# Kernel optimization log

Measured on AMD Instinct MI355X. Metric: run time of the kernel, lower is better.

The kernel has to match this reference:

```python
import jax, jax.numpy as jnp
import numpy as np

VAR_CXCY = 0.1   # variances[0]
VAR_WH = 0.2     # variances[1]
MIN_OVERLAP = 0.5
NEG_POS_RATIO = 3


def cxcy_to_xyxy(b):
    return jnp.concatenate([b[:, :2] - b[:, 2:] / 2, b[:, :2] + b[:, 2:] / 2], axis=-1)


def jaccard(a, b):
    # a: [O,4] xyxy, b: [P,4] xyxy -> [O,P]
    lt = jnp.maximum(a[:, None, :2], b[None, :, :2])
    rb = jnp.minimum(a[:, None, 2:], b[None, :, 2:])
    wh = jnp.clip(rb - lt, 0.0)
    inter = wh[..., 0] * wh[..., 1]
    area_a = (a[:, 2] - a[:, 0]) * (a[:, 3] - a[:, 1])
    area_b = (b[:, 2] - b[:, 0]) * (b[:, 3] - b[:, 1])
    return inter / (area_a[:, None] + area_b[None, :] - inter)


def xyxy_to_gcxgcy(boxes, priors):
    # boxes: [P,4] xyxy matched per-prior; priors: [P,4] cxcywh
    cxcy = (boxes[:, :2] + boxes[:, 2:]) / 2
    wh = boxes[:, 2:] - boxes[:, :2]
    g_cxcy = (cxcy - priors[:, :2]) / (priors[:, 2:] * VAR_CXCY)
    g_wh = jnp.log(wh / priors[:, 2:]) / VAR_WH
    return jnp.concatenate([g_cxcy, g_wh], axis=-1)


def _match_one(boxes, labels, priors, priors_xyxy):
    # boxes: [O,4] xyxy, labels: [O] int
    overlaps = jaccard(boxes, priors_xyxy)          # [O,P]
    prior_overlaps = overlaps.max(axis=0)            # [P]
    prior_objects = overlaps.argmax(axis=0)          # [P]
    object_priors = overlaps.argmax(axis=1)          # [O] best prior per object
    n_obj = boxes.shape[0]
    prior_objects = prior_objects.at[object_priors].set(jnp.arange(n_obj))
    prior_overlaps = prior_overlaps.at[object_priors].set(1.0)
    lab = labels[prior_objects]
    lab = jnp.where(prior_overlaps < MIN_OVERLAP, 0, lab)
    locs = xyxy_to_gcxgcy(boxes[prior_objects], priors)
    return locs, lab


def setup_inputs() -> dict:
    key = jax.random.key(0)
    B, P, C, O = 64, 8732, 81, 16
    ks = jax.random.split(key, 6)
    predict_locs = jax.random.normal(ks[0], (B, P, 4), dtype=jnp.float32)
    predict_confs = jax.random.normal(ks[1], (B, P, C), dtype=jnp.float32)
    # priors in cxcywh, valid sizes
    p_cxcy = jax.random.uniform(ks[2], (P, 2), minval=0.0, maxval=1.0)
    p_wh = jax.random.uniform(ks[2], (P, 2), minval=0.05, maxval=0.3)
    priors = jnp.concatenate([p_cxcy, p_wh], axis=-1).astype(jnp.float32)
    # targets: valid xyxy boxes in [0,1]
    t_cxcy = jax.random.uniform(ks[3], (B, O, 2), minval=0.2, maxval=0.8)
    t_wh = jax.random.uniform(ks[4], (B, O, 2), minval=0.05, maxval=0.4)
    target_boxes = jnp.concatenate([t_cxcy - t_wh / 2, t_cxcy + t_wh / 2], axis=-1).astype(jnp.float32)
    target_labels = jax.random.randint(ks[5], (B, O), 1, C)
    return {
        'predict_locs': predict_locs,
        'predict_confs': predict_confs,
        'target_boxes': target_boxes,
        'target_labels': target_labels,
        'priors': priors,
    }


def reference(predict_locs, predict_confs, target_boxes, target_labels, priors):
    priors_xyxy = cxcy_to_xyxy(priors)
    true_locs, true_confs = jax.vmap(
        lambda b, l: _match_one(b, l, priors, priors_xyxy)
    )(target_boxes, target_labels)              # [B,P,4], [B,P]

    pos = true_confs != 0                        # [B,P]
    n_pos = pos.sum(axis=1)                      # [B]
    n_pos_total = n_pos.sum().astype(predict_locs.dtype)

    # nn.L1Loss(reduction='mean') over the [n_pos_total, 4] gathered entries
    loc_loss = jnp.sum(jnp.abs(predict_locs - true_locs) * pos[..., None]) / (n_pos_total * 4)

    logp = jax.nn.log_softmax(predict_confs, axis=-1)
    ce = -jnp.take_along_axis(logp, true_confs[..., None], axis=-1)[..., 0]  # [B,P]

    ce_pos_sum = jnp.sum(jnp.where(pos, ce, 0.0))
    ce_neg = jnp.where(pos, 0.0, ce)
    # double-sort rank: rank of each prior when sorted by descending neg loss
    rank = jnp.argsort(jnp.argsort(-ce_neg, axis=1), axis=1)
    hard = rank < (NEG_POS_RATIO * n_pos)[:, None]
    ce_hard_sum = jnp.sum(jnp.where(hard, ce_neg, 0.0))

    conf_loss = (ce_hard_sum + ce_pos_sum) / n_pos_total
    return conf_loss + loc_loss
```

## Files before the change

kernel.cpp:

```cpp
#include <hip/hip_runtime.h>
#include <cstdint>
#include <cstddef>

constexpr int O_C   = 16;
constexpr int P_MAX = 8732;
constexpr int CH    = 4;
constexpr int CHP   = 2183;

struct f4u { float x, y, z, w; };

__device__ __forceinline__ float waveSumF(float v) {
    #pragma unroll
    for (int off = 32; off; off >>= 1) v += __shfl_xor(v, off);
    return v;
}
__device__ __forceinline__ int waveSumI(int v) {
    #pragma unroll
    for (int off = 32; off; off >>= 1) v += __shfl_xor(v, off);
    return v;
}

__global__ __launch_bounds__(256) void matchA1(
    const float* __restrict__ target_boxes,
    const float* __restrict__ priors,
    float* __restrict__ ov_out,
    unsigned char* __restrict__ obj_out,
    unsigned long long* __restrict__ okey_part,
    int P)
{
    const int b    = blockIdx.x / CH;
    const int c    = blockIdx.x % CH;
    const int tid  = threadIdx.x;
    const int lane = tid & 63;
    const int wid  = tid >> 6;

    __shared__ float bx0[O_C], by0[O_C], bx1[O_C], by1[O_C], barea[O_C];
    __shared__ unsigned long long s_wb[O_C * 4];

    if (tid < O_C) {
        const float* tb = target_boxes + ((size_t)b * O_C + tid) * 4;
        float x0 = tb[0], y0 = tb[1], x1 = tb[2], y1 = tb[3];
        bx0[tid] = x0; by0[tid] = y0; bx1[tid] = x1; by1[tid] = y1;
        barea[tid] = (x1 - x0) * (y1 - y0);
    }
    __syncthreads();

    float bi[O_C]; int bp[O_C];
    #pragma unroll
    for (int o = 0; o < O_C; ++o) { bi[o] = -1.0f; bp[o] = 0; }

    const int p0 = c * CHP, p1 = min(p0 + CHP, P);
    for (int p = p0 + tid; p < p1; p += 256) {
        float4 pr = reinterpret_cast<const float4*>(priors)[p];
        float px0 = pr.x - pr.z * 0.5f, py0 = pr.y - pr.w * 0.5f;
        float px1 = pr.x + pr.z * 0.5f, py1 = pr.y + pr.w * 0.5f;
        float parea = (px1 - px0) * (py1 - py0);
        float bv = -1.0f; int bo = 0;
        #pragma unroll
        for (int o = 0; o < O_C; ++o) {
            float ix0 = fmaxf(px0, bx0[o]), iy0 = fmaxf(py0, by0[o]);
            float ix1 = fminf(px1, bx1[o]), iy1 = fminf(py1, by1[o]);
            float iw = fmaxf(ix1 - ix0, 0.0f), ih = fmaxf(iy1 - iy0, 0.0f);
            float inter = iw * ih;
            float iou = inter / (barea[o] + parea - inter);
            if (iou > bv) { bv = iou; bo = o; }
            if (iou > bi[o]) { bi[o] = iou; bp[o] = p; }
        }
        ov_out[(size_t)b * P + p]  = bv;
        obj_out[(size_t)b * P + p] = (unsigned char)bo;
    }

    #pragma unroll
    for (int o = 0; o < O_C; ++o) {
        unsigned long long k = (bi[o] >= 0.0f)
            ? (((unsigned long long)__float_as_uint(bi[o]) << 32) |
               (unsigned long long)(0xFFFFFFFFu - (unsigned)bp[o]))
            : 0ull;
        #pragma unroll
        for (int off = 32; off; off >>= 1) {
            unsigned long long k2 = __shfl_xor(k, off);
            if (k2 > k) k = k2;
        }
        if (lane == 0) s_wb[o * 4 + wid] = k;
    }
    __syncthreads();
    if (tid < O_C) {
        unsigned long long k = s_wb[tid * 4];
        #pragma unroll
        for (int w = 1; w < 4; ++w) if (s_wb[tid * 4 + w] > k) k = s_wb[tid * 4 + w];
        okey_part[(size_t)blockIdx.x * O_C + tid] = k;
    }
}

__global__ __launch_bounds__(256) void ce_stream(
    const float* __restrict__ confs,
    const float* __restrict__ ov_in,
    const unsigned char* __restrict__ obj_in,
    const unsigned long long* __restrict__ okey_part,
    const float* __restrict__ target_boxes,
    const int*   __restrict__ target_labels,
    const float* __restrict__ priors,
    const float* __restrict__ predict_locs,
    float* __restrict__ ce_out,
    float* __restrict__ loc_part,
    int P, int rows)
{
    const int tid  = threadIdx.x;
    const int lane = tid & 63;
    const int wid  = tid >> 6;
    const int row0 = blockIdx.x * 256;
    const int row  = row0 + tid;

    __shared__ float4 tbox[2][O_C];
    __shared__ int    tlab[2][O_C], topr[2][O_C];
    __shared__ float  s_facc[4];

    const int b0     = row0 / P;
    const int rsplit = min(row0 + 256, (b0 + 1) * P);
    const int b1     = (rsplit < row0 + 256) ? b0 + 1 : b0;

    if (tid < 2 * O_C) {
        const int seg = tid >> 4, o = tid & 15;
        const int bb  = seg ? b1 : b0;
        const float* tb = target_boxes + ((size_t)bb * O_C + o) * 4;
        tbox[seg][o] = make_float4(tb[0], tb[1], tb[2], tb[3]);
        tlab[seg][o] = target_labels[(size_t)bb * O_C + o];
        unsigned long long kk = 0ull;
        #pragma unroll
        for (int cc = 0; cc < CH; ++cc) {
            unsigned long long k2 = okey_part[((size_t)bb * CH + cc) * O_C + o];
            if (k2 > kk) kk = k2;
        }
        topr[seg][o] = (int)(0xFFFFFFFFu - (unsigned)(kk & 0xFFFFFFFFull));
    }
    __syncthreads();

    const float* rbase = confs + (size_t)row * 81;
    const f4u* rp = reinterpret_cast<const f4u*>(rbase);
    float m = -3.0e38f, s = 0.0f;
    #pragma unroll
    for (int j = 0; j < 20; ++j) {
        f4u a = rp[j];
        float m4 = fmaxf(fmaxf(a.x, a.y), fmaxf(a.z, a.w));
        float mn = fmaxf(m, m4);
        s = s * __expf(m - mn)
          + __expf(a.x - mn) + __expf(a.y - mn)
          + __expf(a.z - mn) + __expf(a.w - mn);
        m = mn;
    }
    {
        float last = rbase[80];
        float mn = fmaxf(m, last);
        s = s * __expf(m - mn) + __expf(last - mn);
        m = mn;
    }

    const int seg = (row >= rsplit) ? 1 : 0;
    const int bb  = seg ? b1 : b0;
    const int p   = row - bb * P;
    float ovv = ov_in[row];
    int   obj = obj_in[row];
    #pragma unroll
    for (int o = 0; o < O_C; ++o)
        if (topr[seg][o] == p) { obj = o; ovv = 1.0f; }
    const int l = (ovv < 0.5f) ? 0 : tlab[seg][obj];

    float xl  = rbase[l];
    float cev = m + __logf(s) - xl;
    ce_out[row] = l ? -cev : cev;

    float locacc = 0.0f;
    if (l) {
        float4 pr = reinterpret_cast<const float4*>(priors)[p];
        float4 tb = tbox[seg][obj];
        float cx = (tb.x + tb.z) * 0.5f, cy = (tb.y + tb.w) * 0.5f;
        float w  = tb.z - tb.x,          h  = tb.w - tb.y;
        float g0 = (cx - pr.x) / (pr.z * 0.1f);
        float g1 = (cy - pr.y) / (pr.w * 0.1f);
        float g2 = logf(w / pr.z) / 0.2f;
        float g3 = logf(h / pr.w) / 0.2f;
        float4 pl = reinterpret_cast<const float4*>(predict_locs)[row];
        locacc = fabsf(pl.x - g0) + fabsf(pl.y - g1) +
                 fabsf(pl.z - g2) + fabsf(pl.w - g3);
    }
    float a = waveSumF(locacc);
    if (lane == 0) s_facc[wid] = a;
    __syncthreads();
    if (tid == 0)
        loc_part[blockIdx.x] = s_facc[0] + s_facc[1] + s_facc[2] + s_facc[3];
}

__global__ __launch_bounds__(1024) void hard_kernel(
    const float* __restrict__ ce,
    int*   __restrict__ n_pos,
    float* __restrict__ ce_pos,
    float* __restrict__ ce_hard,
    int P)
{
    const int b    = blockIdx.x;
    const int tid  = threadIdx.x;
    const int lane = tid & 63;
    const int wid  = tid >> 6;

    __shared__ float s_v[P_MAX];
    __shared__ unsigned int hist[16][256];
    __shared__ unsigned int s_sel;
    __shared__ int s_kr;
    __shared__ float s_f[16], s_f2[16];
    __shared__ int s_i[16];

    const size_t base = (size_t)b * P;
    float possum = 0.0f, negsum = 0.0f;
    int cnt = 0;
    for (int p = tid; p < P; p += 1024) {
        float c = ce[base + p];
        unsigned u = __float_as_uint(c);
        float sv;
        if (u >> 31) { possum += -c; ++cnt; sv = 0.0f; }
        else         { negsum += c;         sv = c;    }
        s_v[p] = sv;
    }
    possum = waveSumF(possum);
    negsum = waveSumF(negsum);
    cnt    = waveSumI(cnt);
    if (lane == 0) { s_f[wid] = possum; s_f2[wid] = negsum; s_i[wid] = cnt; }
    __syncthreads();
    float negsum_t = 0.0f, possum_t = 0.0f; int np = 0;
    #pragma unroll
    for (int w = 0; w < 16; ++w) { negsum_t += s_f2[w]; possum_t += s_f[w]; np += s_i[w]; }
    if (tid == 0) { ce_pos[b] = possum_t; n_pos[b] = np; }

    const int K = 3 * np;
    if (K <= 0) { if (tid == 0) ce_hard[b] = 0.0f; return; }
    if (K >= P) { if (tid == 0) ce_hard[b] = negsum_t; return; }

    unsigned int prefix = 0; int kr = K;
    for (int shift = 24; shift >= 0; shift -= 8) {
        for (int i = tid; i < 16 * 256; i += 1024) (&hist[0][0])[i] = 0;
        __syncthreads();
        unsigned int maskHi = (shift == 24) ? 0u : (0xFFFFFFFFu << (shift + 8));
        for (int p = tid; p < P; p += 1024) {
            unsigned int u = __float_as_uint(s_v[p]);
            if ((u & maskHi) == prefix) atomicAdd(&hist[wid][(u >> shift) & 255], 1u);
        }
        __syncthreads();
        if (wid == 0) {
            unsigned h0 = 0, h1 = 0, h2 = 0, h3 = 0;
            #pragma unroll 4
            for (int w = 0; w < 16; ++w) {
                h0 += hist[w][lane * 4 + 0];
                h1 += hist[w][lane * 4 + 1];
                h2 += hist[w][lane * 4 + 2];
                h3 += hist[w][lane * 4 + 3];
            }
            unsigned own = h0 + h1 + h2 + h3;
            unsigned t = own;
            #pragma unroll
            for (int off = 1; off < 64; off <<= 1) {
                unsigned u = __shfl_down(t, off);
                if (lane + off >= 64) u = 0;
                t += u;
            }
            unsigned Tnext = t - own;
            unsigned cum3 = Tnext;
            unsigned cum2 = cum3 + h3;
            unsigned cum1 = cum2 + h2;
            unsigned cum0 = cum1 + h1;
            unsigned kru = (unsigned)kr;
            int selj = -1; unsigned cg = 0;
            if      (cum3 < kru && kru <= cum3 + h3) { selj = 3; cg = cum3; }
            else if (cum2 < kru && kru <= cum2 + h2) { selj = 2; cg = cum2; }
            else if (cum1 < kru && kru <= cum1 + h1) { selj = 1; cg = cum1; }
            else if (cum0 < kru && kru <= cum0 + h0) { selj = 0; cg = cum0; }
            if (selj >= 0) {
                s_sel = prefix | ((unsigned)(lane * 4 + selj) << shift);
                s_kr  = kr - (int)cg;
            }
        }
        __syncthreads();
        prefix = s_sel; kr = s_kr;
        __syncthreads();
    }

    float sumgt = 0.0f;
    for (int p = tid; p < P; p += 1024) {
        unsigned int u = __float_as_uint(s_v[p]);
        if (u > prefix) sumgt += s_v[p];
    }
    sumgt = waveSumF(sumgt);
    if (lane == 0) s_f[wid] = sumgt;
    __syncthreads();
    if (tid == 0) {
        float sg = 0.0f;
        #pragma unroll
        for (int w = 0; w < 16; ++w) sg += s_f[w];
        ce_hard[b] = sg + (float)kr * __uint_as_float(prefix);
    }
}

__global__ __launch_bounds__(256) void finalize_kernel(
    const int*   __restrict__ n_pos,
    const float* __restrict__ ce_pos,
    const float* __restrict__ ce_hard,
    const float* __restrict__ loc_part,
    float* __restrict__ out, int B, int nblk)
{
    __shared__ float s_f[4];
    __shared__ float s_res[3];
    const int tid  = threadIdx.x;
    const int lane = tid & 63;
    const int wid  = tid >> 6;

    float la = 0.0f;
    for (int i = tid; i < nblk; i += 256) la += loc_part[i];
    la = waveSumF(la);
    if (lane == 0) s_f[wid] = la;

    if (tid < 64) {
        int np = 0; float cp = 0.0f, ch = 0.0f;
        for (int b = lane; b < B; b += 64) {
            np += n_pos[b]; cp += ce_pos[b]; ch += ce_hard[b];
        }
        #pragma unroll
        for (int off = 32; off; off >>= 1) {
            np += __shfl_xor(np, off);
            cp += __shfl_xor(cp, off);
            ch += __shfl_xor(ch, off);
        }
        if (lane == 0) {
            s_res[0] = (float)np; s_res[1] = cp; s_res[2] = ch;
        }
    }
    __syncthreads();
    if (tid == 0) {
        float latot = s_f[0] + s_f[1] + s_f[2] + s_f[3];
        float npt = s_res[0];
        out[0] = (s_res[2] + s_res[1]) / npt + latot / (npt * 4.0f);
    }
}

extern "C" void kernel_launch(void* const* d_in, const int* in_sizes, int n_in,
                              void* d_out, int out_size, void* d_ws, size_t ws_size,
                              hipStream_t stream) {
    const float* predict_locs  = (const float*)d_in[0];
    const float* predict_confs = (const float*)d_in[1];
    const float* target_boxes  = (const float*)d_in[2];
    const int*   target_labels = (const int*)d_in[3];
    const float* priors        = (const float*)d_in[4];

    const int P = in_sizes[4] / 4;
    const int B = in_sizes[0] / (P * 4);
    const int rows = B * P;
    const int nblk = rows / 256;

    char* ws = (char*)d_ws;
    unsigned long long* okey_part = (unsigned long long*)ws;
    ws += (size_t)B * CH * O_C * sizeof(unsigned long long);
    float* ce      = (float*)ws; ws += (size_t)rows * sizeof(float);
    float* ov      = (float*)ws; ws += (size_t)rows * sizeof(float);
    float* loc_p   = (float*)ws; ws += (size_t)nblk * sizeof(float);
    int*   n_pos   = (int*)ws;   ws += (size_t)B * sizeof(int);
    float* ce_pos  = (float*)ws; ws += (size_t)B * sizeof(float);
    float* ce_hard = (float*)ws; ws += (size_t)B * sizeof(float);
    unsigned char* obj = (unsigned char*)ws; ws += (size_t)rows;

    matchA1<<<B * CH, 256, 0, stream>>>(target_boxes, priors, ov, obj, okey_part, P);
    ce_stream<<<nblk, 256, 0, stream>>>(predict_confs, ov, obj, okey_part,
                                        target_boxes, target_labels, priors,
                                        predict_locs, ce, loc_p, P, rows);
    hard_kernel<<<B, 1024, 0, stream>>>(ce, n_pos, ce_pos, ce_hard, P);
    finalize_kernel<<<1, 256, 0, stream>>>(n_pos, ce_pos, ce_hard, loc_p,
                                           (float*)d_out, B, rows / 256);
}
```

Measured before the change: 78.32 us.

## Fuse matching with logsumexp stream and move label/loc work into hard kernel

The prior-matching blocks and the per-row logsumexp blocks now run in one launch, since the logsumexp no longer depends on the match results. Label resolution, the target-logit gather, positive CE and the L1 loc loss move into the per-batch hard-mining kernel, which removes one launch and the serial dependency between matching and the heavy confidence stream. The cost is that the 64-block hard kernel now does scattered gathers from confs and predict_locs, so its low parallelism may lengthen that kernel.

```diff
diff --git a/kernel.cpp b/kernel.cpp
--- a/kernel.cpp
+++ b/kernel.cpp
@@ -20,17 +20,47 @@
     return v;
 }
 
-__global__ __launch_bounds__(256) void matchA1(
+__global__ __launch_bounds__(256, 4) void fused_stream(
+    const float* __restrict__ confs,
     const float* __restrict__ target_boxes,
     const float* __restrict__ priors,
     float* __restrict__ ov_out,
     unsigned char* __restrict__ obj_out,
     unsigned long long* __restrict__ okey_part,
-    int P)
+    float* __restrict__ lse_out,
+    int P, int rows, int nmatch)
 {
-    const int b    = blockIdx.x / CH;
-    const int c    = blockIdx.x % CH;
     const int tid  = threadIdx.x;
+
+    if (blockIdx.x >= nmatch) {
+        const int row = (blockIdx.x - nmatch) * 256 + tid;
+        if (row >= rows) return;
+        const float* rbase = confs + (size_t)row * 81;
+        const f4u* rp = reinterpret_cast<const f4u*>(rbase);
+        float m = -3.0e38f, s = 0.0f;
+        #pragma unroll
+        for (int j = 0; j < 20; ++j) {
+            f4u a = rp[j];
+            float m4 = fmaxf(fmaxf(a.x, a.y), fmaxf(a.z, a.w));
+            float mn = fmaxf(m, m4);
+            s = s * __expf(m - mn)
+              + __expf(a.x - mn) + __expf(a.y - mn)
+              + __expf(a.z - mn) + __expf(a.w - mn);
+            m = mn;
+        }
+        {
+            float last = rbase[80];
+            float mn = fmaxf(m, last);
+            s = s * __expf(m - mn) + __expf(last - mn);
+            m = mn;
+        }
+        lse_out[row] = m + __logf(s);
+        return;
+    }
+
+    const int chunk = blockIdx.x;
+    const int b    = chunk / CH;
+    const int c    = chunk % CH;
     const int lane = tid & 63;
     const int wid  = tid >> 6;
 
@@ -88,12 +118,13 @@
         unsigned long long k = s_wb[tid * 4];
         #pragma unroll
         for (int w = 1; w < 4; ++w) if (s_wb[tid * 4 + w] > k) k = s_wb[tid * 4 + w];
-        okey_part[(size_t)blockIdx.x * O_C + tid] = k;
-    }
-}
-
-__global__ __launch_bounds__(256) void ce_stream(
+        okey_part[(size_t)chunk * O_C + tid] = k;
+    }
+}
+
+__global__ __launch_bounds__(1024) void hard_kernel(
     const float* __restrict__ confs,
+    const float* __restrict__ lse,
     const float* __restrict__ ov_in,
     const unsigned char* __restrict__ obj_in,
     const unsigned long long* __restrict__ okey_part,
@@ -101,100 +132,10 @@
     const int*   __restrict__ target_labels,
     const float* __restrict__ priors,
     const float* __restrict__ predict_locs,
-    float* __restrict__ ce_out,
-    float* __restrict__ loc_part,
-    int P, int rows)
-{
-    const int tid  = threadIdx.x;
-    const int lane = tid & 63;
-    const int wid  = tid >> 6;
-    const int row0 = blockIdx.x * 256;
-    const int row  = row0 + tid;
-
-    __shared__ float4 tbox[2][O_C];
-    __shared__ int    tlab[2][O_C], topr[2][O_C];
-    __shared__ float  s_facc[4];
-
-    const int b0     = row0 / P;
-    const int rsplit = min(row0 + 256, (b0 + 1) * P);
-    const int b1     = (rsplit < row0 + 256) ? b0 + 1 : b0;
-
-    if (tid < 2 * O_C) {
-        const int seg = tid >> 4, o = tid & 15;
-        const int bb  = seg ? b1 : b0;
-        const float* tb = target_boxes + ((size_t)bb * O_C + o) * 4;
-        tbox[seg][o] = make_float4(tb[0], tb[1], tb[2], tb[3]);
-        tlab[seg][o] = target_labels[(size_t)bb * O_C + o];
-        unsigned long long kk = 0ull;
-        #pragma unroll
-        for (int cc = 0; cc < CH; ++cc) {
-            unsigned long long k2 = okey_part[((size_t)bb * CH + cc) * O_C + o];
-            if (k2 > kk) kk = k2;
-        }
-        topr[seg][o] = (int)(0xFFFFFFFFu - (unsigned)(kk & 0xFFFFFFFFull));
-    }
-    __syncthreads();
-
-    const float* rbase = confs + (size_t)row * 81;
-    const f4u* rp = reinterpret_cast<const f4u*>(rbase);
-    float m = -3.0e38f, s = 0.0f;
-    #pragma unroll
-    for (int j = 0; j < 20; ++j) {
-        f4u a = rp[j];
-        float m4 = fmaxf(fmaxf(a.x, a.y), fmaxf(a.z, a.w));
-        float mn = fmaxf(m, m4);
-        s = s * __expf(m - mn)
-          + __expf(a.x - mn) + __expf(a.y - mn)
-          + __expf(a.z - mn) + __expf(a.w - mn);
-        m = mn;
-    }
-    {
-        float last = rbase[80];
-        float mn = fmaxf(m, last);
-        s = s * __expf(m - mn) + __expf(last - mn);
-        m = mn;
-    }
-
-    const int seg = (row >= rsplit) ? 1 : 0;
-    const int bb  = seg ? b1 : b0;
-    const int p   = row - bb * P;
-    float ovv = ov_in[row];
-    int   obj = obj_in[row];
-    #pragma unroll
-    for (int o = 0; o < O_C; ++o)
-        if (topr[seg][o] == p) { obj = o; ovv = 1.0f; }
-    const int l = (ovv < 0.5f) ? 0 : tlab[seg][obj];
-
-    float xl  = rbase[l];
-    float cev = m + __logf(s) - xl;
-    ce_out[row] = l ? -cev : cev;
-
-    float locacc = 0.0f;
-    if (l) {
-        float4 pr = reinterpret_cast<const float4*>(priors)[p];
-        float4 tb = tbox[seg][obj];
-        float cx = (tb.x + tb.z) * 0.5f, cy = (tb.y + tb.w) * 0.5f;
-        float w  = tb.z - tb.x,          h  = tb.w - tb.y;
-        float g0 = (cx - pr.x) / (pr.z * 0.1f);
-        float g1 = (cy - pr.y) / (pr.w * 0.1f);
-        float g2 = logf(w / pr.z) / 0.2f;
-        float g3 = logf(h / pr.w) / 0.2f;
-        float4 pl = reinterpret_cast<const float4*>(predict_locs)[row];
-        locacc = fabsf(pl.x - g0) + fabsf(pl.y - g1) +
-                 fabsf(pl.z - g2) + fabsf(pl.w - g3);
-    }
-    float a = waveSumF(locacc);
-    if (lane == 0) s_facc[wid] = a;
-    __syncthreads();
-    if (tid == 0)
-        loc_part[blockIdx.x] = s_facc[0] + s_facc[1] + s_facc[2] + s_facc[3];
-}
-
-__global__ __launch_bounds__(1024) void hard_kernel(
-    const float* __restrict__ ce,
     int*   __restrict__ n_pos,
     float* __restrict__ ce_pos,
     float* __restrict__ ce_hard,
+    float* __restrict__ loc_b,
     int P)
 {
     const int b    = blockIdx.x;
@@ -204,31 +145,70 @@
 
     __shared__ float s_v[P_MAX];
     __shared__ unsigned int hist[16][256];
+    __shared__ float4 tbox[O_C];
+    __shared__ int    tlab[O_C], topr[O_C];
     __shared__ unsigned int s_sel;
     __shared__ int s_kr;
-    __shared__ float s_f[16], s_f2[16];
+    __shared__ float s_f[16], s_f2[16], s_f3[16];
     __shared__ int s_i[16];
 
+    if (tid < O_C) {
+        const float* tb = target_boxes + ((size_t)b * O_C + tid) * 4;
+        tbox[tid] = make_float4(tb[0], tb[1], tb[2], tb[3]);
+        tlab[tid] = target_labels[(size_t)b * O_C + tid];
+        unsigned long long kk = 0ull;
+        #pragma unroll
+        for (int cc = 0; cc < CH; ++cc) {
+            unsigned long long k2 = okey_part[((size_t)b * CH + cc) * O_C + tid];
+            if (k2 > kk) kk = k2;
+        }
+        topr[tid] = (int)(0xFFFFFFFFu - (unsigned)(kk & 0xFFFFFFFFull));
+    }
+    __syncthreads();
+
     const size_t base = (size_t)b * P;
-    float possum = 0.0f, negsum = 0.0f;
+    float possum = 0.0f, negsum = 0.0f, locsum = 0.0f;
     int cnt = 0;
     for (int p = tid; p < P; p += 1024) {
-        float c = ce[base + p];
-        unsigned u = __float_as_uint(c);
-        float sv;
-        if (u >> 31) { possum += -c; ++cnt; sv = 0.0f; }
-        else         { negsum += c;         sv = c;    }
-        s_v[p] = sv;
+        float ovv = ov_in[base + p];
+        int   obj = obj_in[base + p];
+        #pragma unroll
+        for (int o = 0; o < O_C; ++o)
+            if (topr[o] == p) { obj = o; ovv = 1.0f; }
+        const int l = (ovv < 0.5f) ? 0 : tlab[obj];
+        float xl  = confs[(base + p) * 81 + l];
+        float cev = lse[base + p] - xl;
+        if (l != 0) {
+            possum += cev; ++cnt;
+            s_v[p] = 0.0f;
+            float4 pr = reinterpret_cast<const float4*>(priors)[p];
+            float4 tb = tbox[obj];
+            float cx = (tb.x + tb.z) * 0.5f, cy = (tb.y + tb.w) * 0.5f;
+            float w  = tb.z - tb.x,          h  = tb.w - tb.y;
+            float g0 = (cx - pr.x) / (pr.z * 0.1f);
+            float g1 = (cy - pr.y) / (pr.w * 0.1f);
+            float g2 = logf(w / pr.z) / 0.2f;
+            float g3 = logf(h / pr.w) / 0.2f;
+            float4 pl = reinterpret_cast<const float4*>(predict_locs)[base + p];
+            locsum += fabsf(pl.x - g0) + fabsf(pl.y - g1) +
+                      fabsf(pl.z - g2) + fabsf(pl.w - g3);
+        } else {
+            negsum += cev;
+            s_v[p] = cev;
+        }
     }
     possum = waveSumF(possum);
     negsum = waveSumF(negsum);
+    locsum = waveSumF(locsum);
     cnt    = waveSumI(cnt);
-    if (lane == 0) { s_f[wid] = possum; s_f2[wid] = negsum; s_i[wid] = cnt; }
-    __syncthreads();
-    float negsum_t = 0.0f, possum_t = 0.0f; int np = 0;
-    #pragma unroll
-    for (int w = 0; w < 16; ++w) { negsum_t += s_f2[w]; possum_t += s_f[w]; np += s_i[w]; }
-    if (tid == 0) { ce_pos[b] = possum_t; n_pos[b] = np; }
+    if (lane == 0) { s_f[wid] = possum; s_f2[wid] = negsum; s_f3[wid] = locsum; s_i[wid] = cnt; }
+    __syncthreads();
+    float negsum_t = 0.0f, possum_t = 0.0f, locsum_t = 0.0f; int np = 0;
+    #pragma unroll
+    for (int w = 0; w < 16; ++w) {
+        negsum_t += s_f2[w]; possum_t += s_f[w]; locsum_t += s_f3[w]; np += s_i[w];
+    }
+    if (tid == 0) { ce_pos[b] = possum_t; n_pos[b] = np; loc_b[b] = locsum_t; }
 
     const int K = 3 * np;
     if (K <= 0) { if (tid == 0) ce_hard[b] = 0.0f; return; }
@@ -298,44 +278,28 @@
     }
 }
 
-__global__ __launch_bounds__(256) void finalize_kernel(
+__global__ __launch_bounds__(64) void finalize_kernel(
     const int*   __restrict__ n_pos,
     const float* __restrict__ ce_pos,
     const float* __restrict__ ce_hard,
-    const float* __restrict__ loc_part,
-    float* __restrict__ out, int B, int nblk)
+    const float* __restrict__ loc_b,
+    float* __restrict__ out, int B)
 {
-    __shared__ float s_f[4];
-    __shared__ float s_res[3];
-    const int tid  = threadIdx.x;
-    const int lane = tid & 63;
-    const int wid  = tid >> 6;
-
-    float la = 0.0f;
-    for (int i = tid; i < nblk; i += 256) la += loc_part[i];
-    la = waveSumF(la);
-    if (lane == 0) s_f[wid] = la;
-
-    if (tid < 64) {
-        int np = 0; float cp = 0.0f, ch = 0.0f;
-        for (int b = lane; b < B; b += 64) {
-            np += n_pos[b]; cp += ce_pos[b]; ch += ce_hard[b];
-        }
-        #pragma unroll
-        for (int off = 32; off; off >>= 1) {
-            np += __shfl_xor(np, off);
-            cp += __shfl_xor(cp, off);
-            ch += __shfl_xor(ch, off);
-        }
-        if (lane == 0) {
-            s_res[0] = (float)np; s_res[1] = cp; s_res[2] = ch;
-        }
-    }
-    __syncthreads();
-    if (tid == 0) {
-        float latot = s_f[0] + s_f[1] + s_f[2] + s_f[3];
-        float npt = s_res[0];
-        out[0] = (s_res[2] + s_res[1]) / npt + latot / (npt * 4.0f);
+    const int lane = threadIdx.x;
+    int np = 0; float cp = 0.0f, ch = 0.0f, la = 0.0f;
+    for (int b = lane; b < B; b += 64) {
+        np += n_pos[b]; cp += ce_pos[b]; ch += ce_hard[b]; la += loc_b[b];
+    }
+    #pragma unroll
+    for (int off = 32; off; off >>= 1) {
+        np += __shfl_xor(np, off);
+        cp += __shfl_xor(cp, off);
+        ch += __shfl_xor(ch, off);
+        la += __shfl_xor(la, off);
+    }
+    if (lane == 0) {
+        float npt = (float)np;
+        out[0] = (ch + cp) / npt + la / (npt * 4.0f);
     }
 }
 
@@ -351,24 +315,26 @@
     const int P = in_sizes[4] / 4;
     const int B = in_sizes[0] / (P * 4);
     const int rows = B * P;
-    const int nblk = rows / 256;
+    const int nmatch = B * CH;
+    const int nlse = rows / 256;
 
     char* ws = (char*)d_ws;
     unsigned long long* okey_part = (unsigned long long*)ws;
-    ws += (size_t)B * CH * O_C * sizeof(unsigned long long);
-    float* ce      = (float*)ws; ws += (size_t)rows * sizeof(float);
+    ws += (size_t)nmatch * O_C * sizeof(unsigned long long);
+    float* lse     = (float*)ws; ws += (size_t)rows * sizeof(float);
     float* ov      = (float*)ws; ws += (size_t)rows * sizeof(float);
-    float* loc_p   = (float*)ws; ws += (size_t)nblk * sizeof(float);
     int*   n_pos   = (int*)ws;   ws += (size_t)B * sizeof(int);
     float* ce_pos  = (float*)ws; ws += (size_t)B * sizeof(float);
     float* ce_hard = (float*)ws; ws += (size_t)B * sizeof(float);
+    float* loc_b   = (float*)ws; ws += (size_t)B * sizeof(float);
     unsigned char* obj = (unsigned char*)ws; ws += (size_t)rows;
 
-    matchA1<<<B * CH, 256, 0, stream>>>(target_boxes, priors, ov, obj, okey_part, P);
-    ce_stream<<<nblk, 256, 0, stream>>>(predict_confs, ov, obj, okey_part,
-                                        target_boxes, target_labels, priors,
-                                        predict_locs, ce, loc_p, P, rows);
-    hard_kernel<<<B, 1024, 0, stream>>>(ce, n_pos, ce_pos, ce_hard, P);
-    finalize_kernel<<<1, 256, 0, stream>>>(n_pos, ce_pos, ce_hard, loc_p,
-                                           (float*)d_out, B, rows / 256);
-}
+    fused_stream<<<nmatch + nlse, 256, 0, stream>>>(
+        predict_confs, target_boxes, priors, ov, obj, okey_part, lse,
+        P, rows, nmatch);
+    hard_kernel<<<B, 1024, 0, stream>>>(
+        predict_confs, lse, ov, obj, okey_part, target_boxes, target_labels,
+        priors, predict_locs, n_pos, ce_pos, ce_hard, loc_b, P);
+    finalize_kernel<<<1, 64, 0, stream>>>(n_pos, ce_pos, ce_hard, loc_b,
+                                          (float*)d_out, B);
+}
```

After: 106.3 us. 35.8% more time.
